# Kernel tuning notes

Hardware: AMD Instinct MI355X
Metric: run time of the kernel (lower is better)

The kernel has to match this reference:

```python
import jax, jax.numpy as jnp
import numpy as np
from jax import lax

MODES1, MODES2 = 16, 16
WIDTH = 64
T_IN, T_OUT = 10, 40
STATE, PAR = 1, 2
PAD = 9  # self.padding in FNO2d


def setup_inputs() -> dict:
    key = jax.random.key(0)
    ks = jax.random.split(key, 12)
    B, S = 32, 512
    u = jax.random.normal(ks[0], (B, S, T_IN), jnp.float32)
    x = jax.random.uniform(ks[1], (B, S), jnp.float32)
    t = jax.random.uniform(ks[2], (B, T_OUT), jnp.float32)
    par = jax.random.normal(ks[3], (B, PAR), jnp.float32)
    cin = T_IN + PAR + 2
    fc0_w = jax.random.normal(ks[4], (cin, WIDTH), jnp.float32) * 0.1
    fc0_b = jnp.zeros((WIDTH,), jnp.float32)
    scale = 1.0 / (WIDTH * WIDTH)
    spec_wr = jax.random.uniform(ks[5], (4, WIDTH, WIDTH, MODES1, MODES2), jnp.float32) * scale
    spec_wi = jax.random.uniform(ks[6], (4, WIDTH, WIDTH, MODES1, MODES2), jnp.float32) * scale
    w_conv = jax.random.normal(ks[7], (4, WIDTH, WIDTH), jnp.float32) * 0.05
    w_bias = jnp.zeros((4, WIDTH), jnp.float32)
    fc1_w = jax.random.normal(ks[8], (WIDTH, 128), jnp.float32) * 0.05
    fc1_b = jnp.zeros((128,), jnp.float32)
    fc2_w = jax.random.normal(ks[9], (128, STATE), jnp.float32) * 0.05
    fc2_b = jnp.zeros((STATE,), jnp.float32)
    return dict(u=u, x=x, t=t, par=par, fc0_w=fc0_w, fc0_b=fc0_b,
                spec_wr=spec_wr, spec_wi=spec_wi, w_conv=w_conv, w_bias=w_bias,
                fc1_w=fc1_w, fc1_b=fc1_b, fc2_w=fc2_w, fc2_b=fc2_b)


def _spectral_conv(v, wr, wi):
    # v: [B, Cin, X, T] real; wr/wi: [Cin, Cout, m1, m2]
    B, C, X, T = v.shape
    w = lax.complex(wr, wi)
    v_ft = jnp.fft.rfftn(v, axes=(2, 3))                      # [B, Cin, X, T//2+1] complex64
    corner = jnp.einsum('bixt,ioxt->boxt', v_ft[:, :, :MODES1, :MODES2], w)
    out_ft = jnp.zeros((B, w.shape[1], X, T // 2 + 1), jnp.complex64)
    out_ft = out_ft.at[:, :, :MODES1, :MODES2].set(corner)
    return jnp.fft.irfftn(out_ft, s=(X, T), axes=(2, 3))


def reference(u, x, t, par, fc0_w, fc0_b, spec_wr, spec_wi, w_conv, w_bias,
              fc1_w, fc1_b, fc2_w, fc2_b):
    B, S = u.shape[0], u.shape[1]
    # assemble (u repeated over T_out, par broadcast, grid (x, t)) -> [B,S,T_out,cin]
    uu = jnp.broadcast_to(u[:, :, None, :], (B, S, T_OUT, T_IN))
    pp = jnp.broadcast_to(par[:, None, None, :], (B, S, T_OUT, PAR))
    gx = jnp.broadcast_to(x[:, :, None, None], (B, S, T_OUT, 1))
    gt = jnp.broadcast_to(t[:, None, :, None], (B, S, T_OUT, 1))
    v = jnp.concatenate([uu, pp, gx, gt], axis=-1)
    v = v @ fc0_w + fc0_b                                      # [B,S,T_out,W]
    v = jnp.transpose(v, (0, 3, 1, 2))                         # [B,W,S,T_out]
    v = jnp.pad(v, ((0, 0), (0, 0), (0, PAD), (0, PAD)))       # pad right on x and t
    for i in range(4):
        u1 = _spectral_conv(v, spec_wr[i], spec_wi[i])
        u2 = jnp.einsum('bcxt,oc->boxt', v, w_conv[i]) + w_bias[i][None, :, None, None]
        v = u1 + u2
        if i < 3:
            v = jax.nn.gelu(v, approximate=False)
    v = v[:, :, :-PAD, :-PAD]
    v = jnp.transpose(v, (0, 2, 3, 1))                         # [B,S,T_out,W]
    v = jax.nn.gelu(v @ fc1_w + fc1_b, approximate=False)
    return v @ fc2_w + fc2_b                                   # [B,S,T_out,STATE]
```

## Files before the change

### kernel.cpp

```cpp
#include <hip/hip_runtime.h>
#include <math.h>

#define XDIM 521
#define TDIM 49
#define TPAD 52
#define XT (XDIM*TPAD)
#define NBTOT 32
#define NC 64
#define NS 512
#define NTO 40
#define NTIN 10
#define CIN 14
#define PI_D 3.14159265358979323846

__device__ __forceinline__ float gelu_f(float x){
  return 0.5f*x*(1.0f + erff(x*0.70710678118654752440f));
}

__device__ __forceinline__ float gelu_fast(float x){
  float z = x*0.70710678118654752440f;
  float az = fabsf(z);
  float t = __frcp_rn(fmaf(0.3275911f, az, 1.0f));
  float p = fmaf(1.061405429f, t, -1.453152027f);
  p = fmaf(p, t, 1.421413741f);
  p = fmaf(p, t, -0.284496736f);
  p = fmaf(p, t, 0.254829592f);
  p = p*t;
  float e = __expf(-az*az);
  float erfa = fmaf(-p, e, 1.0f);
  float erfz = (z < 0.f) ? -erfa : erfa;
  return 0.5f*x*(1.0f + erfz);
}

__global__ void k_init(float* __restrict__ TXC, float* __restrict__ TXS,
                       float* __restrict__ TTC, float* __restrict__ TTS,
                       float* __restrict__ ITC, float* __restrict__ ITS,
                       float* __restrict__ WT0, float* __restrict__ WT1, float* __restrict__ WTC,
                       const float* __restrict__ fc0_w, const float* __restrict__ fc1_w,
                       const float* __restrict__ w_conv){
  int i = blockIdx.x*256 + threadIdx.x;
  if (i < XDIM*16){
    int x = i >> 4, kx = i & 15;
    double ang = 2.0*PI_D*(double)((x*kx)%XDIM)/(double)XDIM;
    TXC[i] = (float)cos(ang);
    TXS[i] = (float)sin(ang);
  }
  if (i < TDIM*16){
    int t = i >> 4, kt = i & 15;
    double ang = 2.0*PI_D*(double)((t*kt)%TDIM)/(double)TDIM;
    TTC[i] = (float)cos(ang);
    TTS[i] = (float)sin(ang);
    double nrm = ((kt==0)?1.0:2.0)/(double)(XDIM*TDIM);
    ITC[i] = (float)(nrm*cos(ang));
    ITS[i] = (float)(nrm*sin(ang));
  }
  if (i < 64*16){
    int c = i >> 4, k = i & 15;
    WT0[i] = (k < CIN) ? fc0_w[k*64 + c] : 0.f;
  }
  if (i < 128*64){
    int j = i >> 6, c = i & 63;
    WT1[i] = fc1_w[c*128 + j];
  }
  if (i < 4*64*64){
    int l = i >> 12, r = i & 4095, c = r >> 6, o = r & 63;
    WTC[i] = w_conv[(l*64 + o)*64 + c];
  }
}

__global__ void k_fc0(const float* __restrict__ u, const float* __restrict__ xg,
                      const float* __restrict__ tg, const float* __restrict__ par,
                      const float* __restrict__ WT0, const float* __restrict__ fc0_b,
                      float* __restrict__ v, int b0){
  int bl = blockIdx.y;
  int b  = b0 + bl;
  int p = blockIdx.x*256 + threadIdx.x;
  if (p >= XT) return;
  int x = p / TPAD, t = p - x*TPAD;
  bool valid = (x < NS) && (t < NTO);
  float in[CIN];
  if (valid){
    #pragma unroll
    for (int k=0;k<NTIN;k++) in[k] = u[((size_t)(b*NS+x))*NTIN + k];
    in[10] = par[b*2+0]; in[11] = par[b*2+1];
    in[12] = xg[b*NS + x];
    in[13] = tg[b*NTO + t];
  } else {
    #pragma unroll
    for (int k=0;k<CIN;k++) in[k] = 0.f;
  }
  size_t base = ((size_t)bl*NC)*XT + p;
  for (int c=0;c<NC;c++){
    float acc = valid ? fc0_b[c] : 0.f;
    #pragma unroll
    for (int k=0;k<CIN;k++) acc = fmaf(in[k], WT0[c*16+k], acc);
    v[base + (size_t)c*XT] = acc;
  }
}

__device__ __forceinline__ void dft_reduce_emit(
    float (&ar)[16], float (&ai)[16], int w, int t,
    const float* __restrict__ TTC, const float* __restrict__ TTS,
    float* __restrict__ cVR, float* __restrict__ cVI, int bo, int NCB){
  __shared__ float redR[4*16*50], redI[4*16*50];
  if (t < TDIM){
    #pragma unroll
    for (int kx=0;kx<16;kx++){
      redR[(w*16+kx)*50 + t] = ar[kx];
      redI[(w*16+kx)*50 + t] = ai[kx];
    }
  }
  __syncthreads();
  int tid = w*64 + t;
  for (int q = tid; q < 784; q += 256){
    int kx = q/49, tt = q - kx*49;
    int idx = kx*50 + tt;
    float sR = redR[idx] + redR[800+idx] + redR[1600+idx] + redR[2400+idx];
    float sI = redI[idx] + redI[800+idx] + redI[1600+idx] + redI[2400+idx];
    redR[idx] = sR; redI[idx] = sI;
  }
  __syncthreads();
  int kx = tid >> 4, kt = tid & 15;
  float accR=0.f, accI=0.f;
  for (int tt=0; tt<TDIM; tt++){
    float vr = redR[kx*50+tt], vi = redI[kx*50+tt];
    float c = TTC[tt*16+kt], s = TTS[tt*16+kt];
    accR += vr*c + vi*s;
    accI += vi*c - vr*s;
  }
  cVR[(size_t)tid*NCB + bo] = accR;
  cVI[(size_t)tid*NCB + bo] = accI;
}

__global__ void __launch_bounds__(256) k_dftxt(const float* __restrict__ v,
    const float* __restrict__ TXC, const float* __restrict__ TXS,
    const float* __restrict__ TTC, const float* __restrict__ TTS,
    float* __restrict__ cVR0, float* __restrict__ cVI0,
    float* __restrict__ cVR1, float* __restrict__ cVI1, int NCB){
  int bo = blockIdx.x >> 1, h = blockIdx.x & 1;
  int w = threadIdx.x >> 6, t = threadIdx.x & 63;
  bool act = (t < TDIM);
  const float* vp = v + (size_t)bo*XT + (act ? t : 0);
  float ar[16], ai[16];
  #pragma unroll
  for (int k=0;k<16;k++){ ar[k]=0.f; ai[k]=0.f; }
  if (h == 0 && w == 0){
    float v0 = act ? vp[0] : 0.f;
    #pragma unroll
    for (int k=0;k<16;k++) ar[k] += v0;
  }
  int chunk = h*4 + w;
  int p0 = 1 + (chunk*65)/2, p1 = 1 + ((chunk+1)*65)/2;
  for (int p=p0; p<p1; p++){
    int xa = p, xb = XDIM - p;
    float va = act ? vp[xa*TPAD] : 0.f;
    float vbv= act ? vp[xb*TPAD] : 0.f;
    float sp = va + vbv, sm = va - vbv;
    const float4 tc0 = *reinterpret_cast<const float4*>(TXC + xa*16 + 0);
    const float4 tc1 = *reinterpret_cast<const float4*>(TXC + xa*16 + 4);
    const float4 tc2 = *reinterpret_cast<const float4*>(TXC + xa*16 + 8);
    const float4 tc3 = *reinterpret_cast<const float4*>(TXC + xa*16 + 12);
    const float4 ts0 = *reinterpret_cast<const float4*>(TXS + xa*16 + 0);
    const float4 ts1 = *reinterpret_cast<const float4*>(TXS + xa*16 + 4);
    const float4 ts2 = *reinterpret_cast<const float4*>(TXS + xa*16 + 8);
    const float4 ts3 = *reinterpret_cast<const float4*>(TXS + xa*16 + 12);
    ar[0]  = fmaf(sp, tc0.x, ar[0]);  ai[0]  = fmaf(-sm, ts0.x, ai[0]);
    ar[1]  = fmaf(sp, tc0.y, ar[1]);  ai[1]  = fmaf(-sm, ts0.y, ai[1]);
    ar[2]  = fmaf(sp, tc0.z, ar[2]);  ai[2]  = fmaf(-sm, ts0.z, ai[2]);
    ar[3]  = fmaf(sp, tc0.w, ar[3]);  ai[3]  = fmaf(-sm, ts0.w, ai[3]);
    ar[4]  = fmaf(sp, tc1.x, ar[4]);  ai[4]  = fmaf(-sm, ts1.x, ai[4]);
    ar[5]  = fmaf(sp, tc1.y, ar[5]);  ai[5]  = fmaf(-sm, ts1.y, ai[5]);
    ar[6]  = fmaf(sp, tc1.z, ar[6]);  ai[6]  = fmaf(-sm, ts1.z, ai[6]);
    ar[7]  = fmaf(sp, tc1.w, ar[7]);  ai[7]  = fmaf(-sm, ts1.w, ai[7]);
    ar[8]  = fmaf(sp, tc2.x, ar[8]);  ai[8]  = fmaf(-sm, ts2.x, ai[8]);
    ar[9]  = fmaf(sp, tc2.y, ar[9]);  ai[9]  = fmaf(-sm, ts2.y, ai[9]);
    ar[10] = fmaf(sp, tc2.z, ar[10]); ai[10] = fmaf(-sm, ts2.z, ai[10]);
    ar[11] = fmaf(sp, tc2.w, ar[11]); ai[11] = fmaf(-sm, ts2.w, ai[11]);
    ar[12] = fmaf(sp, tc3.x, ar[12]); ai[12] = fmaf(-sm, ts3.x, ai[12]);
    ar[13] = fmaf(sp, tc3.y, ar[13]); ai[13] = fmaf(-sm, ts3.y, ai[13]);
    ar[14] = fmaf(sp, tc3.z, ar[14]); ai[14] = fmaf(-sm, ts3.z, ai[14]);
    ar[15] = fmaf(sp, tc3.w, ar[15]); ai[15] = fmaf(-sm, ts3.w, ai[15]);
  }
  dft_reduce_emit(ar, ai, w, t, TTC, TTS, h ? cVR1 : cVR0, h ? cVI1 : cVI0, bo, NCB);
}

__global__ void k_spec(const float* __restrict__ swr, const float* __restrict__ swi,
                       const float* __restrict__ cVR0, const float* __restrict__ cVI0,
                       const float* __restrict__ cVR1, const float* __restrict__ cVI1,
                       float* __restrict__ cOR, float* __restrict__ cOI, int l, int NCB){
  int m = blockIdx.x;
  __shared__ float wr[4096], wi[4096];
  __shared__ float vr[32*65], vi[32*65];
  const size_t wb = (size_t)l*64*64*256 + m;
  for (int q = threadIdx.x; q < 4096; q += 256){
    wr[q] = swr[wb + (size_t)q*256];
    wi[q] = swi[wb + (size_t)q*256];
  }
  for (int q = threadIdx.x; q < NCB; q += 256){
    int b=q>>6, i=q&63;
    vr[b*65+i] = cVR0[(size_t)m*NCB+q] + cVR1[(size_t)m*NCB+q];
    vi[b*65+i] = cVI0[(size_t)m*NCB+q] + cVI1[(size_t)m*NCB+q];
  }
  __syncthreads();
  int b = threadIdx.x >> 3, og = threadIdx.x & 7;
  if (b*64 < NCB){
    float oR[8], oI[8];
    #pragma unroll
    for (int j=0;j<8;j++){ oR[j]=0.f; oI[j]=0.f; }
    for (int i=0;i<64;i++){
      float arv = vr[b*65+i], aiv = vi[b*65+i];
      #pragma unroll
      for (int j=0;j<8;j++){
        float wrv = wr[i*64 + og*8 + j], wiv = wi[i*64 + og*8 + j];
        oR[j] = fmaf(arv,wrv,fmaf(-aiv,wiv,oR[j]));
        oI[j] = fmaf(arv,wiv,fmaf( aiv,wrv,oI[j]));
      }
    }
    #pragma unroll
    for (int j=0;j<8;j++){
      cOR[(size_t)m*NCB + b*64 + og*8 + j] = oR[j];
      cOI[(size_t)m*NCB + b*64 + og*8 + j] = oI[j];
    }
  }
}

__global__ void __launch_bounds__(256) k_invG(const float* __restrict__ cOR, const float* __restrict__ cOI,
    const float* __restrict__ ITC, const float* __restrict__ ITS,
    float* __restrict__ GR, float* __restrict__ GI, int NCB){
  int bo = blockIdx.x;
  __shared__ float lcr[256], lci[256];
  int q = threadIdx.x;
  lcr[q] = cOR[(size_t)q*NCB + bo];
  lci[q] = cOI[(size_t)q*NCB + bo];
  __syncthreads();
  int kx = q >> 4, tq = q & 15;
  for (int t = tq; t < TDIM; t += 16){
    float gr=0.f, gi=0.f;
    #pragma unroll
    for (int kt=0;kt<16;kt++){
      float cr = lcr[kx*16+kt], ci = lci[kx*16+kt];
      float wc = ITC[t*16+kt], ws = ITS[t*16+kt];
      gr = fmaf(cr,wc,fmaf(-ci,ws,gr));
      gi = fmaf(cr,ws,fmaf( ci,wc,gi));
    }
    GR[(size_t)bo*784 + kx*TDIM + t] = gr;
    GI[(size_t)bo*784 + kx*TDIM + t] = gi;
  }
}

__global__ void __launch_bounds__(256) k_conv(float* __restrict__ v,
    const float* __restrict__ WTC, const float* __restrict__ w_bias, int l){
  int bl = blockIdx.y;
  int p = blockIdx.x*512 + threadIdx.x*2;
  if (p >= XT) return;
  const float* wl = WTC + l*4096;
  float a0[64], a1[64];
  #pragma unroll
  for (int o=0;o<64;o++){ a0[o]=0.f; a1[o]=0.f; }
  const size_t bb = (size_t)bl*NC*XT;
  for (int c=0;c<NC;c++){
    const float2 vv = *reinterpret_cast<const float2*>(v + bb + (size_t)c*XT + p);
    #pragma unroll
    for (int o=0;o<64;o++){
      float wv = wl[c*64+o];
      a0[o] = fmaf(vv.x, wv, a0[o]);
      a1[o] = fmaf(vv.y, wv, a1[o]);
    }
  }
  #pragma unroll
  for (int o=0;o<64;o++){
    float bias = w_bias[l*64+o];
    float2 rr; rr.x = a0[o]+bias; rr.y = a1[o]+bias;
    *reinterpret_cast<float2*>(v + bb + (size_t)o*XT + p) = rr;
  }
}

template<int GELU, int EMIT>
__global__ void __launch_bounds__(256) k_inv2dft(const float* __restrict__ GR, const float* __restrict__ GI,
    const float* __restrict__ TXC, const float* __restrict__ TXS,
    const float* __restrict__ TTC, const float* __restrict__ TTS,
    float* __restrict__ v,
    float* __restrict__ cVR0, float* __restrict__ cVI0,
    float* __restrict__ cVR1, float* __restrict__ cVI1, int NCB){
  int bo = blockIdx.x >> 1, h = blockIdx.x & 1;
  int w = threadIdx.x >> 6, t = threadIdx.x & 63;
  bool act = (t < TDIM);
  int tcl = act ? t : 0;
  float gr[16], gi[16];
  #pragma unroll
  for (int kx=0;kx<16;kx++){
    gr[kx] = GR[(size_t)bo*784 + kx*TDIM + tcl];
    gi[kx] = GI[(size_t)bo*784 + kx*TDIM + tcl];
  }
  float ar[16], ai[16];
  #pragma unroll
  for (int k=0;k<16;k++){ ar[k]=0.f; ai[k]=0.f; }
  float* vb = v + (size_t)bo*XT;
  if (h == 0 && w == 0){
    float s1 = 0.f;
    #pragma unroll
    for (int k=0;k<16;k++) s1 += gr[k];
    float r = 0.f;
    if (act){
      r = s1 + vb[t];
      if (GELU) r = gelu_fast(r);
    }
    if (t < TPAD) vb[t] = r;
    if (EMIT){
      #pragma unroll
      for (int k=0;k<16;k++) ar[k] += r;
    }
  }
  int chunk = h*4 + w;
  int p0 = 1 + (chunk*65)/2, p1 = 1 + ((chunk+1)*65)/2;
  for (int p=p0; p<p1; p++){
    int xa = p, xb = XDIM - p;
    const float4 tc0 = *reinterpret_cast<const float4*>(TXC + xa*16 + 0);
    const float4 tc1 = *reinterpret_cast<const float4*>(TXC + xa*16 + 4);
    const float4 tc2 = *reinterpret_cast<const float4*>(TXC + xa*16 + 8);
    const float4 tc3 = *reinterpret_cast<const float4*>(TXC + xa*16 + 12);
    const float4 ts0 = *reinterpret_cast<const float4*>(TXS + xa*16 + 0);
    const float4 ts1 = *reinterpret_cast<const float4*>(TXS + xa*16 + 4);
    const float4 ts2 = *reinterpret_cast<const float4*>(TXS + xa*16 + 8);
    const float4 ts3 = *reinterpret_cast<const float4*>(TXS + xa*16 + 12);
    float s1, s2;
    s1  = gr[0]*tc0.x;             s2  = gi[0]*ts0.x;
    s1  = fmaf(gr[1],  tc0.y, s1); s2  = fmaf(gi[1],  ts0.y, s2);
    s1  = fmaf(gr[2],  tc0.z, s1); s2  = fmaf(gi[2],  ts0.z, s2);
    s1  = fmaf(gr[3],  tc0.w, s1); s2  = fmaf(gi[3],  ts0.w, s2);
    s1  = fmaf(gr[4],  tc1.x, s1); s2  = fmaf(gi[4],  ts1.x, s2);
    s1  = fmaf(gr[5],  tc1.y, s1); s2  = fmaf(gi[5],  ts1.y, s2);
    s1  = fmaf(gr[6],  tc1.z, s1); s2  = fmaf(gi[6],  ts1.z, s2);
    s1  = fmaf(gr[7],  tc1.w, s1); s2  = fmaf(gi[7],  ts1.w, s2);
    s1  = fmaf(gr[8],  tc2.x, s1); s2  = fmaf(gi[8],  ts2.x, s2);
    s1  = fmaf(gr[9],  tc2.y, s1); s2  = fmaf(gi[9],  ts2.y, s2);
    s1  = fmaf(gr[10], tc2.z, s1); s2  = fmaf(gi[10], ts2.z, s2);
    s1  = fmaf(gr[11], tc2.w, s1); s2  = fmaf(gi[11], ts2.w, s2);
    s1  = fmaf(gr[12], tc3.x, s1); s2  = fmaf(gi[12], ts3.x, s2);
    s1  = fmaf(gr[13], tc3.y, s1); s2  = fmaf(gi[13], ts3.y, s2);
    s1  = fmaf(gr[14], tc3.z, s1); s2  = fmaf(gi[14], ts3.z, s2);
    s1  = fmaf(gr[15], tc3.w, s1); s2  = fmaf(gi[15], ts3.w, s2);
    float accA = s1 - s2, accB = s1 + s2;
    float rA = 0.f, rB = 0.f;
    if (act){
      rA = accA + vb[(size_t)xa*TPAD + t];
      rB = accB + vb[(size_t)xb*TPAD + t];
      if (GELU){ rA = gelu_fast(rA); rB = gelu_fast(rB); }
    }
    if (t < TPAD){
      vb[(size_t)xa*TPAD + t] = rA;
      vb[(size_t)xb*TPAD + t] = rB;
    }
    if (EMIT){
      float sp = rA + rB, sm = rA - rB;
      ar[0]  = fmaf(sp, tc0.x, ar[0]);  ai[0]  = fmaf(-sm, ts0.x, ai[0]);
      ar[1]  = fmaf(sp, tc0.y, ar[1]);  ai[1]  = fmaf(-sm, ts0.y, ai[1]);
      ar[2]  = fmaf(sp, tc0.z, ar[2]);  ai[2]  = fmaf(-sm, ts0.z, ai[2]);
      ar[3]  = fmaf(sp, tc0.w, ar[3]);  ai[3]  = fmaf(-sm, ts0.w, ai[3]);
      ar[4]  = fmaf(sp, tc1.x, ar[4]);  ai[4]  = fmaf(-sm, ts1.x, ai[4]);
      ar[5]  = fmaf(sp, tc1.y, ar[5]);  ai[5]  = fmaf(-sm, ts1.y, ai[5]);
      ar[6]  = fmaf(sp, tc1.z, ar[6]);  ai[6]  = fmaf(-sm, ts1.z, ai[6]);
      ar[7]  = fmaf(sp, tc1.w, ar[7]);  ai[7]  = fmaf(-sm, ts1.w, ai[7]);
      ar[8]  = fmaf(sp, tc2.x, ar[8]);  ai[8]  = fmaf(-sm, ts2.x, ai[8]);
      ar[9]  = fmaf(sp, tc2.y, ar[9]);  ai[9]  = fmaf(-sm, ts2.y, ai[9]);
      ar[10] = fmaf(sp, tc2.z, ar[10]); ai[10] = fmaf(-sm, ts2.z, ai[10]);
      ar[11] = fmaf(sp, tc2.w, ar[11]); ai[11] = fmaf(-sm, ts2.w, ai[11]);
      ar[12] = fmaf(sp, tc3.x, ar[12]); ai[12] = fmaf(-sm, ts3.x, ai[12]);
      ar[13] = fmaf(sp, tc3.y, ar[13]); ai[13] = fmaf(-sm, ts3.y, ai[13]);
      ar[14] = fmaf(sp, tc3.z, ar[14]); ai[14] = fmaf(-sm, ts3.z, ai[14]);
      ar[15] = fmaf(sp, tc3.w, ar[15]); ai[15] = fmaf(-sm, ts3.w, ai[15]);
    }
  }
  if (EMIT) dft_reduce_emit(ar, ai, w, t, TTC, TTS, h ? cVR1 : cVR0, h ? cVI1 : cVI0, bo, NCB);
}

__global__ void k_final(const float* __restrict__ v, const float* __restrict__ WT1,
                        const float* __restrict__ fc1_b, const float* __restrict__ fc2_w,
                        const float* __restrict__ fc2_b, float* __restrict__ out, int b0){
  int bl = blockIdx.y;
  int pp = blockIdx.x*256 + threadIdx.x;
  int s = pp / NTO, to = pp - s*NTO;
  float vr[64];
  size_t vb = (size_t)bl*NC*XT + (size_t)s*TPAD + to;
  #pragma unroll
  for (int c=0;c<64;c++) vr[c] = v[vb + (size_t)c*XT];
  float accA = fc2_b[0], accB = 0.f;
  for (int j=0;j<128;j++){
    const float* wj = WT1 + j*64;
    float h0 = fc1_b[j], h1 = 0.f, h2 = 0.f, h3 = 0.f;
    #pragma unroll
    for (int c=0;c<64;c+=4){
      h0 = fmaf(vr[c+0], wj[c+0], h0);
      h1 = fmaf(vr[c+1], wj[c+1], h1);
      h2 = fmaf(vr[c+2], wj[c+2], h2);
      h3 = fmaf(vr[c+3], wj[c+3], h3);
    }
    float h = (h0+h1)+(h2+h3);
    h = gelu_fast(h);
    if (j & 1) accB = fmaf(h, fc2_w[j], accB);
    else       accA = fmaf(h, fc2_w[j], accA);
  }
  out[((size_t)(b0+bl))*20480 + pp] = accA + accB;
}

extern "C" void kernel_launch(void* const* d_in, const int* in_sizes, int n_in,
                              void* d_out, int out_size, void* d_ws, size_t ws_size,
                              hipStream_t stream){
  const float* u     = (const float*)d_in[0];
  const float* xg    = (const float*)d_in[1];
  const float* tg    = (const float*)d_in[2];
  const float* par   = (const float*)d_in[3];
  const float* fc0_w = (const float*)d_in[4];
  const float* fc0_b = (const float*)d_in[5];
  const float* swr   = (const float*)d_in[6];
  const float* swi   = (const float*)d_in[7];
  const float* wconv = (const float*)d_in[8];
  const float* wbias = (const float*)d_in[9];
  const float* fc1_w = (const float*)d_in[10];
  const float* fc1_b = (const float*)d_in[11];
  const float* fc2_w = (const float*)d_in[12];
  const float* fc2_b = (const float*)d_in[13];

  int nb = NBTOT;
  while (nb > 1){
    size_t need = (45408ull + (size_t)nb*64ull*29684ull) * 4ull;
    if (need <= ws_size) break;
    nb >>= 1;
  }
  const int NCB = nb*64;

  float* W = (float*)d_ws;
  size_t off = 0;
  float* TXC = W + off; off += 8336;
  float* TXS = W + off; off += 8336;
  float* TTC = W + off; off += 784;
  float* TTS = W + off; off += 784;
  float* ITC = W + off; off += 784;
  float* ITS = W + off; off += 784;
  float* WT0 = W + off; off += 1024;
  float* WT1 = W + off; off += 8192;
  float* WTC = W + off; off += 16384;
  float* VA  = W + off; off += (size_t)NCB*XT;
  float* VXR = W + off; off += (size_t)NCB*784;
  float* VXI = W + off; off += (size_t)NCB*784;
  float* CVR = W + off; off += (size_t)256*NCB;
  float* CVI = W + off; off += (size_t)256*NCB;
  float* COR = W + off; off += (size_t)256*NCB;
  float* COI = W + off; off += (size_t)256*NCB;

  k_init<<<64, 256, 0, stream>>>(TXC,TXS,TTC,TTS,ITC,ITS,WT0,WT1,WTC, fc0_w, fc1_w, wconv);

  const int nch = NBTOT / nb;
  for (int ch = 0; ch < nch; ch++){
    int b0 = ch*nb;
    k_fc0<<<dim3((XT+255)/256, nb), 256, 0, stream>>>(u, xg, tg, par, WT0, fc0_b, VA, b0);
    k_dftxt<<<NCB*2, 256, 0, stream>>>(VA, TXC, TXS, TTC, TTS, CVR, CVI, COR, COI, NCB);
    for (int l=0; l<4; l++){
      k_spec<<<256, 256, 0, stream>>>(swr, swi, CVR, CVI, COR, COI, COR, COI, l, NCB);
      k_invG<<<NCB, 256, 0, stream>>>(COR, COI, ITC, ITS, VXR, VXI, NCB);
      k_conv<<<dim3(53, nb), 256, 0, stream>>>(VA, WTC, wbias, l);
      if (l < 3) k_inv2dft<1,1><<<NCB*2, 256, 0, stream>>>(VXR, VXI, TXC, TXS, TTC, TTS, VA, CVR, CVI, COR, COI, NCB);
      else       k_inv2dft<0,0><<<NCB*2, 256, 0, stream>>>(VXR, VXI, TXC, TXS, TTC, TTS, VA, CVR, CVI, COR, COI, NCB);
    }
    k_final<<<dim3(80, nb), 256, 0, stream>>>(VA, WT1, fc1_b, fc2_w, fc2_b, (float*)d_out, b0);
  }
}
```

Measured before the change: 1.827 ms.

## Compute final fc1 projection with split-bf16 MFMA instead of scalar FMAs

The final fc1+gelu+fc2 kernel now runs the 64x128 projection on matrix cores using bf16 MFMA 16x16x32. Both operands are split into high and low bf16 parts, and three MFMAs per K-step approximate fp32 precision. The weights are pre-packed in MFMA lane order during init. Each wave handles 16 points, the fc2 dot is reduced with cross-lane shuffles, and the grid grows to four times as many blocks. The cost is extra conversion work and some precision loss, traded against the scalar FMA cost of the old per-thread loop, which held 64 registers of activations.

```diff
diff --git a/kernel.cpp b/kernel.cpp
--- a/kernel.cpp
+++ b/kernel.cpp
@@ -13,8 +13,17 @@
 #define CIN 14
 #define PI_D 3.14159265358979323846
 
-__device__ __forceinline__ float gelu_f(float x){
-  return 0.5f*x*(1.0f + erff(x*0.70710678118654752440f));
+typedef __attribute__((ext_vector_type(8))) short bf16x8;
+typedef __attribute__((ext_vector_type(4))) float f32x4;
+typedef unsigned short ushort_t;
+
+__device__ __forceinline__ ushort_t f2bf(float x){
+  union { float f; unsigned int u; } a; a.f = x;
+  unsigned int r = a.u + 0x7FFF + ((a.u >> 16) & 1);
+  return (ushort_t)(r >> 16);
+}
+__device__ __forceinline__ float bf2f(ushort_t h){
+  union { unsigned int u; float f; } a; a.u = ((unsigned int)h) << 16; return a.f;
 }
 
 __device__ __forceinline__ float gelu_fast(float x){
@@ -36,6 +45,7 @@
                        float* __restrict__ TTC, float* __restrict__ TTS,
                        float* __restrict__ ITC, float* __restrict__ ITS,
                        float* __restrict__ WT0, float* __restrict__ WT1, float* __restrict__ WTC,
+                       ushort_t* __restrict__ AH, ushort_t* __restrict__ AL,
                        const float* __restrict__ fc0_w, const float* __restrict__ fc1_w,
                        const float* __restrict__ w_conv){
   int i = blockIdx.x*256 + threadIdx.x;
@@ -65,6 +75,16 @@
   if (i < 4*64*64){
     int l = i >> 12, r = i & 4095, c = r >> 6, o = r & 63;
     WTC[i] = w_conv[(l*64 + o)*64 + c];
+  }
+  if (i < 8192){
+    int ii = i & 7, lane = (i >> 3) & 63, kjt = i >> 9;
+    int jt = kjt >> 1, ks = kjt & 1;
+    int j = jt*16 + (lane & 15);
+    int c = ks*32 + (lane >> 4)*8 + ii;
+    float wv = fc1_w[c*128 + j];
+    ushort_t hi = f2bf(wv);
+    AH[i] = hi;
+    AL[i] = f2bf(wv - bf2f(hi));
   }
 }
 
@@ -374,33 +394,54 @@
   if (EMIT) dft_reduce_emit(ar, ai, w, t, TTC, TTS, h ? cVR1 : cVR0, h ? cVI1 : cVI0, bo, NCB);
 }
 
-__global__ void k_final(const float* __restrict__ v, const float* __restrict__ WT1,
-                        const float* __restrict__ fc1_b, const float* __restrict__ fc2_w,
-                        const float* __restrict__ fc2_b, float* __restrict__ out, int b0){
+__global__ void __launch_bounds__(256) k_final(const float* __restrict__ v,
+    const ushort_t* __restrict__ AH, const ushort_t* __restrict__ AL,
+    const float* __restrict__ fc1_b, const float* __restrict__ fc2_w,
+    const float* __restrict__ fc2_b, float* __restrict__ out, int b0){
   int bl = blockIdx.y;
-  int pp = blockIdx.x*256 + threadIdx.x;
+  int wv = threadIdx.x >> 6, l = threadIdx.x & 63;
+  int col = l & 15, g = l >> 4;
+  int tile = blockIdx.x*4 + wv;
+  int pp = tile*16 + col;
   int s = pp / NTO, to = pp - s*NTO;
-  float vr[64];
-  size_t vb = (size_t)bl*NC*XT + (size_t)s*TPAD + to;
-  #pragma unroll
-  for (int c=0;c<64;c++) vr[c] = v[vb + (size_t)c*XT];
-  float accA = fc2_b[0], accB = 0.f;
-  for (int j=0;j<128;j++){
-    const float* wj = WT1 + j*64;
-    float h0 = fc1_b[j], h1 = 0.f, h2 = 0.f, h3 = 0.f;
-    #pragma unroll
-    for (int c=0;c<64;c+=4){
-      h0 = fmaf(vr[c+0], wj[c+0], h0);
-      h1 = fmaf(vr[c+1], wj[c+1], h1);
-      h2 = fmaf(vr[c+2], wj[c+2], h2);
-      h3 = fmaf(vr[c+3], wj[c+3], h3);
-    }
-    float h = (h0+h1)+(h2+h3);
-    h = gelu_fast(h);
-    if (j & 1) accB = fmaf(h, fc2_w[j], accB);
-    else       accA = fmaf(h, fc2_w[j], accA);
-  }
-  out[((size_t)(b0+bl))*20480 + pp] = accA + accB;
+  const float* vb = v + (size_t)bl*NC*XT + (size_t)s*TPAD + to;
+  bf16x8 Bh[2], Bl[2];
+  #pragma unroll
+  for (int ks=0; ks<2; ks++){
+    #pragma unroll
+    for (int i=0; i<8; i++){
+      int c = ks*32 + g*8 + i;
+      float x = vb[(size_t)c*XT];
+      ushort_t hi = f2bf(x);
+      ushort_t lo = f2bf(x - bf2f(hi));
+      Bh[ks][i] = (short)hi;
+      Bl[ks][i] = (short)lo;
+    }
+  }
+  float partial = 0.f;
+  #pragma unroll
+  for (int jt=0; jt<8; jt++){
+    f32x4 acc = {0.f, 0.f, 0.f, 0.f};
+    #pragma unroll
+    for (int ks=0; ks<2; ks++){
+      int aidx = ((jt*2 + ks)*64 + l)*8;
+      bf16x8 Ah = *reinterpret_cast<const bf16x8*>(AH + aidx);
+      bf16x8 Al = *reinterpret_cast<const bf16x8*>(AL + aidx);
+      acc = __builtin_amdgcn_mfma_f32_16x16x32_bf16(Ah, Bh[ks], acc, 0, 0, 0);
+      acc = __builtin_amdgcn_mfma_f32_16x16x32_bf16(Ah, Bl[ks], acc, 0, 0, 0);
+      acc = __builtin_amdgcn_mfma_f32_16x16x32_bf16(Al, Bh[ks], acc, 0, 0, 0);
+    }
+    #pragma unroll
+    for (int reg=0; reg<4; reg++){
+      int j = jt*16 + g*4 + reg;
+      float hh = acc[reg] + fc1_b[j];
+      hh = gelu_fast(hh);
+      partial = fmaf(hh, fc2_w[j], partial);
+    }
+  }
+  partial += __shfl_xor(partial, 16, 64);
+  partial += __shfl_xor(partial, 32, 64);
+  if (g == 0) out[((size_t)(b0+bl))*20480 + pp] = partial + fc2_b[0];
 }
 
 extern "C" void kernel_launch(void* const* d_in, const int* in_sizes, int n_in,
@@ -423,7 +464,7 @@
 
   int nb = NBTOT;
   while (nb > 1){
-    size_t need = (45408ull + (size_t)nb*64ull*29684ull) * 4ull;
+    size_t need = (53600ull + (size_t)nb*64ull*29684ull) * 4ull;
     if (need <= ws_size) break;
     nb >>= 1;
   }
@@ -440,6 +481,8 @@
   float* WT0 = W + off; off += 1024;
   float* WT1 = W + off; off += 8192;
   float* WTC = W + off; off += 16384;
+  ushort_t* AH = (ushort_t*)(W + off); off += 4096;
+  ushort_t* AL = (ushort_t*)(W + off); off += 4096;
   float* VA  = W + off; off += (size_t)NCB*XT;
   float* VXR = W + off; off += (size_t)NCB*784;
   float* VXI = W + off; off += (size_t)NCB*784;
@@ -448,7 +491,7 @@
   float* COR = W + off; off += (size_t)256*NCB;
   float* COI = W + off; off += (size_t)256*NCB;
 
-  k_init<<<64, 256, 0, stream>>>(TXC,TXS,TTC,TTS,ITC,ITS,WT0,WT1,WTC, fc0_w, fc1_w, wconv);
+  k_init<<<64, 256, 0, stream>>>(TXC,TXS,TTC,TTS,ITC,ITS,WT0,WT1,WTC, AH, AL, fc0_w, fc1_w, wconv);
 
   const int nch = NBTOT / nb;
   for (int ch = 0; ch < nch; ch++){
@@ -462,6 +505,6 @@
       if (l < 3) k_inv2dft<1,1><<<NCB*2, 256, 0, stream>>>(VXR, VXI, TXC, TXS, TTC, TTS, VA, CVR, CVI, COR, COI, NCB);
       else       k_inv2dft<0,0><<<NCB*2, 256, 0, stream>>>(VXR, VXI, TXC, TXS, TTC, TTS, VA, CVR, CVI, COR, COI, NCB);
     }
-    k_final<<<dim3(80, nb), 256, 0, stream>>>(VA, WT1, fc1_b, fc2_w, fc2_b, (float*)d_out, b0);
-  }
-}
+    k_final<<<dim3(320, nb), 256, 0, stream>>>(VA, AH, AL, fc1_b, fc2_w, fc2_b, (float*)d_out, b0);
+  }
+}
```

Result: faster. 1.716 ms (-6.1%).
